# Kernel tuning notes

Measured on AMD Instinct MI355X. Metric: run time of the kernel, lower is better.

## Reference

```python
import jax, jax.numpy as jnp
import numpy as np

EPS = 1e-7  # tf.keras.backend.epsilon()
NUM_HEADS = 8


def setup_inputs() -> dict:
    key = jax.random.key(0)
    ks = jax.random.split(key, 7)
    B, H, W, C = 4, 128, 128, 512
    glorot = (2.0 / (C + C)) ** 0.5
    x = jax.random.normal(ks[0], (B, H, W, C), dtype=jnp.float32)
    wq = jax.random.normal(ks[1], (C, C), dtype=jnp.float32) * glorot
    bq = jnp.zeros((C,), dtype=jnp.float32)
    wk = jax.random.normal(ks[2], (C, C), dtype=jnp.float32) * glorot
    bk = jnp.zeros((C,), dtype=jnp.float32)
    wv = jax.random.normal(ks[3], (C, C), dtype=jnp.float32) * glorot
    bv = jnp.zeros((C,), dtype=jnp.float32)
    return {"x": x, "wq": wq, "bq": bq, "wk": wk, "bk": bk, "wv": wv, "bv": bv}


def _axial_attention(query, key, value, num_heads):
    B, H, W, C = value.shape
    d = query.shape[-1] // num_heads
    q5 = query.reshape(B, H, W, num_heads, d)
    k5 = key.reshape(B, H, W, num_heads, d)
    # column (vertical) attention: scores over H, per column w -> [B, nh, W, H, H]
    v_att = jnp.einsum("bhwnd,bgwnd->bnwhg", q5, k5)
    # row (horizontal) attention: scores over W, per row h -> [B, nh, H, W, W]
    u_att = jnp.einsum("bhwnd,bhvnd->bnhwv", q5, k5)
    # faithful clip-before-softmax chain from the original module
    v_att = jnp.clip(v_att, -1.0 + EPS, 1.0 - EPS)
    u_att = jnp.clip(u_att, -1.0 + EPS, 1.0 - EPS)
    scale = jnp.sqrt(jnp.asarray(d, dtype=v_att.dtype))
    v_att = v_att / scale
    u_att = u_att / scale
    # safed_softmax: softmax in fp32 (inputs already fp32 here)
    v_att = jax.nn.softmax(v_att.astype(jnp.float32), axis=-1).astype(query.dtype)
    u_att = jax.nn.softmax(u_att.astype(jnp.float32), axis=-1).astype(query.dtype)
    v_att = jnp.where(jnp.isnan(v_att), EPS, v_att)
    u_att = jnp.where(jnp.isnan(u_att), EPS, u_att)
    v_att = jnp.clip(v_att, EPS, 1.0 - EPS)
    u_att = jnp.clip(u_att, EPS, 1.0 - EPS)
    # value: [B, nh, W, H, d]
    val5 = value.reshape(B, H, W, num_heads, d)
    xv = jnp.einsum("bnwhg,bnwgd->bnhwd", v_att, val5.transpose(0, 3, 2, 1, 4))
    xu = jnp.einsum("bnhwv,bnhvd->bnhwd", u_att, xv)
    # transpose (0,2,3,4,1): head index becomes last -> channels ordered [d, nh]
    out = xu.transpose(0, 2, 3, 4, 1).reshape(B, H, W, d * num_heads)
    return out


def reference(x, wq, bq, wk, bk, wv, bv):
    # 1x1 convs == per-pixel dense projections
    query = jnp.einsum("bhwc,cf->bhwf", x, wq) + bq
    key = jnp.einsum("bhwc,cf->bhwf", x, wk) + bk
    value = jnp.einsum("bhwc,cf->bhwf", x, wv) + bv
    return _axial_attention(query, key, value, NUM_HEADS)
```

## Files before the change

kernel.cpp:

```cpp
#include <hip/hip_runtime.h>

typedef unsigned short ush;
typedef __attribute__((ext_vector_type(8))) __bf16 bf16x8;
typedef __attribute__((ext_vector_type(4))) float f32x4;

#define NE 33554432L

__device__ __forceinline__ float b2f(ush u) {
  return __uint_as_float(((unsigned int)u) << 16);
}
__device__ __forceinline__ ush f2b(float f) {
  unsigned int x = __float_as_uint(f);
  x += 0x7fffu + ((x >> 16) & 1u);
  return (ush)(x >> 16);
}
__device__ __forceinline__ bf16x8 bc8(int4 v) { return __builtin_bit_cast(bf16x8, v); }

__device__ __forceinline__ void gload16(const ush* g, ush* l) {
  __builtin_amdgcn_global_load_lds(
      (const __attribute__((address_space(1))) void*)g,
      (__attribute__((address_space(3))) void*)l, 16, 0, 0);
}

__global__ __launch_bounds__(256)
void detect_dtype(const ush* __restrict__ x, int* __restrict__ flag) {
  __shared__ int red[256];
  const int t = threadIdx.x;
  int cnt = 0;
  for (int i = t; i < 16384; i += 256) {
    const int e = (x[i] >> 7) & 0xFF;
    cnt += (e == 0 || (e >= 100 && e <= 142)) ? 1 : 0;
  }
  red[t] = cnt;
  __syncthreads();
  for (int s = 128; s > 0; s >>= 1) {
    if (t < s) red[t] += red[t + s];
    __syncthreads();
  }
  if (t == 0) flag[0] = (red[0] >= 13107) ? 1 : 0;
}

__global__ __launch_bounds__(256)
void pack_x(const void* __restrict__ xin, ush* __restrict__ xb,
            const int* __restrict__ flag) {
  const long i0 = ((long)blockIdx.x * 256 + threadIdx.x) * 8;
  if (*flag) {
    *(int4*)&xb[i0] = *(const int4*)&((const ush*)xin)[i0];
  } else {
    const float* xf = (const float*)xin;
    const float4 a = *(const float4*)&xf[i0];
    const float4 b = *(const float4*)&xf[i0 + 4];
    union { ush u[8]; int4 v; } r;
    r.u[0] = f2b(a.x); r.u[1] = f2b(a.y); r.u[2] = f2b(a.z); r.u[3] = f2b(a.w);
    r.u[4] = f2b(b.x); r.u[5] = f2b(b.y); r.u[6] = f2b(b.z); r.u[7] = f2b(b.w);
    *(int4*)&xb[i0] = r.v;
  }
}

__global__ __launch_bounds__(256)
void pack_w(const void* __restrict__ w0, const void* __restrict__ w1,
            const void* __restrict__ w2, ush* __restrict__ wTb,
            const int* __restrict__ flag) {
  __shared__ ush tile[32][33];
  const void* w = (blockIdx.z == 0) ? w0 : ((blockIdx.z == 1) ? w1 : w2);
  ush* wT = wTb + (long)blockIdx.z * 262144;
  const int bx = blockIdx.x * 32, by = blockIdx.y * 32;
  const int tx = threadIdx.x & 31, ty = threadIdx.x >> 5;
  const int f = *flag;
#pragma unroll
  for (int j = 0; j < 32; j += 8) {
    const int k = by + ty + j, n = bx + tx;
    tile[ty + j][tx] = f ? ((const ush*)w)[k * 512 + n]
                         : f2b(((const float*)w)[k * 512 + n]);
  }
  __syncthreads();
#pragma unroll
  for (int j = 0; j < 32; j += 8)
    wT[(bx + ty + j) * 512 + by + tx] = tile[tx][ty + j];
}

__global__ void pack_bias(const void* __restrict__ b0, const void* __restrict__ b1,
                          const void* __restrict__ b2, float* __restrict__ biasf,
                          const int* __restrict__ flag) {
  const void* b = (blockIdx.x == 0) ? b0 : ((blockIdx.x == 1) ? b1 : b2);
  const int n = threadIdx.x;
  const float v = (*flag) ? b2f(((const ush*)b)[n]) : ((const float*)b)[n];
  biasf[blockIdx.x * 512 + n] = v;
}

__global__ __launch_bounds__(256)
void proj_gemm(const ush* __restrict__ xb, const ush* __restrict__ wTb,
               const float* __restrict__ biasf, ush* __restrict__ qkv) {
  __shared__ ush As[4096];
  __shared__ ush Bs[4096];

  const int z = blockIdx.z;
  const ush* wt = wTb + (long)z * 262144;
  const float* bias = biasf + z * 512;
  ush* out = qkv + (long)z * NE;

  const int t = threadIdx.x;
  const int lane = t & 63;
  const int wvid = t >> 6;
  const int wm = wvid & 1, wn = wvid >> 1;
  const int col = lane & 15, quad = lane >> 4;

  const long m0 = (long)blockIdx.y * 128;
  const int n0 = blockIdx.x * 128;

  const int r_in_g = lane >> 2;
  const int swz = (((lane & 3) ^ ((r_in_g >> 1) & 3)) * 8);
  const int g0 = wvid * 2, g1 = g0 + 1;
  const ush* gA0 = xb + (m0 + g0 * 16 + r_in_g) * 512 + swz;
  const ush* gA1 = xb + (m0 + g1 * 16 + r_in_g) * 512 + swz;
  const ush* gB0 = wt + (long)(n0 + g0 * 16 + r_in_g) * 512 + swz;
  const ush* gB1 = wt + (long)(n0 + g1 * 16 + r_in_g) * 512 + swz;
  ush* lA0 = &As[g0 * 512];
  ush* lA1 = &As[g1 * 512];
  ush* lB0 = &Bs[g0 * 512];
  ush* lB1 = &Bs[g1 * 512];

  const int kswz = ((quad ^ ((col >> 1) & 3)) * 8);
  int aofs[4], bofs[4];
#pragma unroll
  for (int i = 0; i < 4; i++) aofs[i] = (wm * 64 + i * 16 + col) * 32 + kswz;
#pragma unroll
  for (int j = 0; j < 4; j++) bofs[j] = (wn * 64 + j * 16 + col) * 32 + kswz;

  const f32x4 z4 = {0.f, 0.f, 0.f, 0.f};
  f32x4 acc[4][4];
#pragma unroll
  for (int i = 0; i < 4; i++)
#pragma unroll
    for (int j = 0; j < 4; j++) acc[i][j] = z4;

  for (int k0 = 0; k0 < 512; k0 += 32) {
    gload16(gA0 + k0, lA0);
    gload16(gA1 + k0, lA1);
    gload16(gB0 + k0, lB0);
    gload16(gB1 + k0, lB1);
    __syncthreads();
    bf16x8 a[4], b[4];
#pragma unroll
    for (int i = 0; i < 4; i++) a[i] = bc8(*(const int4*)&As[aofs[i]]);
#pragma unroll
    for (int j = 0; j < 4; j++) b[j] = bc8(*(const int4*)&Bs[bofs[j]]);
#pragma unroll
    for (int i = 0; i < 4; i++)
#pragma unroll
      for (int j = 0; j < 4; j++)
        acc[i][j] = __builtin_amdgcn_mfma_f32_16x16x32_bf16(a[i], b[j], acc[i][j], 0, 0, 0);
    __syncthreads();
  }

#pragma unroll
  for (int j = 0; j < 4; j++) {
    const int n = n0 + wn * 64 + j * 16 + col;
    const float bb = bias[n];
#pragma unroll
    for (int i = 0; i < 4; i++) {
      const long row0 = m0 + wm * 64 + i * 16 + quad * 4;
#pragma unroll
      for (int r = 0; r < 4; r++)
        out[(row0 + r) * 512 + n] = f2b(acc[i][j][r] + bb);
    }
  }
}

#define QS_STRIDE 72
#define VT_STRIDE 136
#define P_STRIDE  136

__device__ __forceinline__ int vt_idx(int d, int g) {
  return d * VT_STRIDE + ((((g >> 3) ^ ((d >> 3) & 7)) << 3) | (g & 7));
}

template<int PASS>
__global__ __launch_bounds__(256, 3)
void axial_attn_mfma(const ush* __restrict__ Qb, const ush* __restrict__ Kb,
                     ush* __restrict__ Vb, void* __restrict__ outp,
                     const int* __restrict__ flagp) {
  __shared__ ush smem[27136];
  ush* Qs = smem;
  ush* Ks = smem + 9216;
  ush* Vt = smem + 18432;
  ush* P  = smem;

  const int flg = *flagp;
  const int b = blockIdx.z, n = blockIdx.y, pp = blockIdx.x;
  long base; int stride;
  if (PASS == 1) { base = ((long)b * 16384 + pp) * 512 + n * 64; stride = 65536; }
  else           { base = ((long)(b * 128 + pp) * 128) * 512 + n * 64; stride = 512; }

  const int t = threadIdx.x;
#pragma unroll
  for (int it = 0; it < 4; it++) {
    const int c = t + it * 256;
    const int row = c >> 3, c8 = c & 7;
    const long g = base + (long)row * stride + c8 * 8;
    int4 q = *(const int4*)(Qb + g);
    int4 k = *(const int4*)(Kb + g);
    int4 v = *(const int4*)(Vb + g);
    *(int4*)&Qs[row * QS_STRIDE + c8 * 8] = q;
    *(int4*)&Ks[row * QS_STRIDE + c8 * 8] = k;
    union { int4 i4; ush u[8]; } vu; vu.i4 = v;
#pragma unroll
    for (int dd = 0; dd < 8; dd++)
      Vt[vt_idx(c8 * 8 + dd, row)] = vu.u[dd];
  }
  __syncthreads();

  const int lane = t & 63, wv = t >> 6;
  const int col = lane & 15, quad = lane >> 4;
  const int m0 = wv * 32;
  const f32x4 z4 = {0.f, 0.f, 0.f, 0.f};

  f32x4 sacc[2][8];
#pragma unroll
  for (int i = 0; i < 2; i++)
#pragma unroll
    for (int j = 0; j < 8; j++) sacc[i][j] = z4;
#pragma unroll
  for (int k0 = 0; k0 < 64; k0 += 32) {
    bf16x8 a[2], kb[8];
#pragma unroll
    for (int i = 0; i < 2; i++)
      a[i] = bc8(*(const int4*)&Qs[(m0 + i * 16 + col) * QS_STRIDE + k0 + quad * 8]);
#pragma unroll
    for (int j = 0; j < 8; j++)
      kb[j] = bc8(*(const int4*)&Ks[(j * 16 + col) * QS_STRIDE + k0 + quad * 8]);
#pragma unroll
    for (int i = 0; i < 2; i++)
#pragma unroll
      for (int j = 0; j < 8; j++)
        sacc[i][j] = __builtin_amdgcn_mfma_f32_16x16x32_bf16(a[i], kb[j], sacc[i][j], 0, 0, 0);
  }

  const float CLIP = 1.0f - 1e-7f;
  float e[2][8][4], inv[2][4];
#pragma unroll
  for (int i = 0; i < 2; i++)
#pragma unroll
    for (int r = 0; r < 4; r++) {
      float part = 0.f;
#pragma unroll
      for (int j = 0; j < 8; j++) {
        float s = sacc[i][j][r];
        s = fminf(fmaxf(s, -CLIP), CLIP) * 0.125f;
        const float ee = __expf(s);
        e[i][j][r] = ee;
        part += ee;
      }
      part += __shfl_xor(part, 1);
      part += __shfl_xor(part, 2);
      part += __shfl_xor(part, 4);
      part += __shfl_xor(part, 8);
      inv[i][r] = 1.0f / part;
    }
  __syncthreads();

#pragma unroll
  for (int i = 0; i < 2; i++)
#pragma unroll
    for (int r = 0; r < 4; r++) {
      const int row = m0 + i * 16 + quad * 4 + r;
#pragma unroll
      for (int j = 0; j < 8; j++) {
        const float pv = fminf(fmaxf(e[i][j][r] * inv[i][r], 1e-7f), CLIP);
        P[row * P_STRIDE + j * 16 + col] = f2b(pv);
      }
    }
  __syncthreads();

  f32x4 oacc[2][4];
#pragma unroll
  for (int i = 0; i < 2; i++)
#pragma unroll
    for (int j = 0; j < 4; j++) oacc[i][j] = z4;
#pragma unroll
  for (int k0 = 0; k0 < 128; k0 += 32) {
    bf16x8 a[2], vb[4];
#pragma unroll
    for (int i = 0; i < 2; i++)
      a[i] = bc8(*(const int4*)&P[(m0 + i * 16 + col) * P_STRIDE + k0 + quad * 8]);
#pragma unroll
    for (int j = 0; j < 4; j++)
      vb[j] = bc8(*(const int4*)&Vt[vt_idx(j * 16 + col, k0 + quad * 8)]);
#pragma unroll
    for (int i = 0; i < 2; i++)
#pragma unroll
      for (int j = 0; j < 4; j++)
        oacc[i][j] = __builtin_amdgcn_mfma_f32_16x16x32_bf16(a[i], vb[j], oacc[i][j], 0, 0, 0);
  }

#pragma unroll
  for (int i = 0; i < 2; i++)
#pragma unroll
    for (int r = 0; r < 4; r++) {
      const int row = m0 + i * 16 + quad * 4 + r;
#pragma unroll
      for (int j = 0; j < 4; j++) {
        const int d = j * 16 + col;
        const float val = oacc[i][j][r];
        if (PASS == 1) {
          Vb[base + (long)row * stride + d] = f2b(val);
        } else {
          const long oi = ((long)(b * 128 + pp) * 128 + row) * 512 + d * 8 + n;
          if (flg) ((ush*)outp)[oi] = f2b(val);
          else     ((float*)outp)[oi] = val;
        }
      }
    }
}

extern "C" void kernel_launch(void* const* d_in, const int* in_sizes, int n_in,
                              void* d_out, int out_size, void* d_ws, size_t ws_size,
                              hipStream_t stream) {
  const void* x  = d_in[0];
  const void* wq = d_in[1];
  const void* bq = d_in[2];
  const void* wk = d_in[3];
  const void* bk = d_in[4];
  const void* wv = d_in[5];
  const void* bv = d_in[6];

  char* ws = (char*)d_ws;
  int*   flag  = (int*)ws;
  float* biasf = (float*)(ws + 256);
  ush*   wTb   = (ush*)(ws + 8192);
  ush*   xb    = (ush*)(ws + 8192 + 1572864);
  ush*   qkv   = (ush*)(ws + 8192 + 1572864 + 67108864);

  dim3 blk(256);
  detect_dtype<<<1, blk, 0, stream>>>((const ush*)x, flag);
  pack_bias<<<3, 512, 0, stream>>>(bq, bk, bv, biasf, flag);
  pack_w<<<dim3(16, 16, 3), blk, 0, stream>>>(wq, wk, wv, wTb, flag);
  pack_x<<<16384, blk, 0, stream>>>(x, xb, flag);

  ush* Q = qkv;
  ush* K = Q + NE;
  ush* V = K + NE;
  proj_gemm<<<dim3(4, 512, 3), blk, 0, stream>>>(xb, wTb, biasf, Q);
  dim3 agrid(128, 8, 4);
  axial_attn_mfma<1><<<agrid, blk, 0, stream>>>(Q, K, V, d_out, flag);
  axial_attn_mfma<2><<<agrid, blk, 0, stream>>>(Q, K, V, d_out, flag);
}
```

Baseline: 681.3 us.

## Double-buffer projection GEMM, coalesce attention stores, add output interleave kernel

The projection GEMM now double-buffers its LDS tiles and prefetches the next K slice while the current one is being multiplied. The attention kernel raises wave priority around its MFMA loops. Pass 1 stages its output through LDS so V is written with coalesced 16-byte stores. Pass 2 writes a contiguous fp32 scratch tensor, reusing the xb workspace, and a new out_interleave kernel transposes it into the strided [d, nh] channel layout through LDS, processed in two batch halves. This targets the scattered per-element output writes at the cost of extra scratch traffic and more kernel launches.

```diff
diff --git a/kernel.cpp b/kernel.cpp
--- a/kernel.cpp
+++ b/kernel.cpp
@@ -91,8 +91,8 @@
 __global__ __launch_bounds__(256)
 void proj_gemm(const ush* __restrict__ xb, const ush* __restrict__ wTb,
                const float* __restrict__ biasf, ush* __restrict__ qkv) {
-  __shared__ ush As[4096];
-  __shared__ ush Bs[4096];
+  __shared__ ush As[2][4096];
+  __shared__ ush Bs[2][4096];
 
   const int z = blockIdx.z;
   const ush* wt = wTb + (long)z * 262144;
@@ -115,17 +115,13 @@
   const ush* gA1 = xb + (m0 + g1 * 16 + r_in_g) * 512 + swz;
   const ush* gB0 = wt + (long)(n0 + g0 * 16 + r_in_g) * 512 + swz;
   const ush* gB1 = wt + (long)(n0 + g1 * 16 + r_in_g) * 512 + swz;
-  ush* lA0 = &As[g0 * 512];
-  ush* lA1 = &As[g1 * 512];
-  ush* lB0 = &Bs[g0 * 512];
-  ush* lB1 = &Bs[g1 * 512];
 
   const int kswz = ((quad ^ ((col >> 1) & 3)) * 8);
-  int aofs[4], bofs[4];
+  int aofs[4], bofs4[4];
 #pragma unroll
   for (int i = 0; i < 4; i++) aofs[i] = (wm * 64 + i * 16 + col) * 32 + kswz;
 #pragma unroll
-  for (int j = 0; j < 4; j++) bofs[j] = (wn * 64 + j * 16 + col) * 32 + kswz;
+  for (int j = 0; j < 4; j++) bofs4[j] = (wn * 64 + j * 16 + col) * 32 + kswz;
 
   const f32x4 z4 = {0.f, 0.f, 0.f, 0.f};
   f32x4 acc[4][4];
@@ -134,23 +130,34 @@
 #pragma unroll
     for (int j = 0; j < 4; j++) acc[i][j] = z4;
 
+  gload16(gA0, &As[0][g0 * 512]);
+  gload16(gA1, &As[0][g1 * 512]);
+  gload16(gB0, &Bs[0][g0 * 512]);
+  gload16(gB1, &Bs[0][g1 * 512]);
+  __syncthreads();
+
+  int cur = 0;
   for (int k0 = 0; k0 < 512; k0 += 32) {
-    gload16(gA0 + k0, lA0);
-    gload16(gA1 + k0, lA1);
-    gload16(gB0 + k0, lB0);
-    gload16(gB1 + k0, lB1);
-    __syncthreads();
+    const int nk = k0 + 32;
+    if (nk < 512) {
+      const int nb = cur ^ 1;
+      gload16(gA0 + nk, &As[nb][g0 * 512]);
+      gload16(gA1 + nk, &As[nb][g1 * 512]);
+      gload16(gB0 + nk, &Bs[nb][g0 * 512]);
+      gload16(gB1 + nk, &Bs[nb][g1 * 512]);
+    }
     bf16x8 a[4], b[4];
 #pragma unroll
-    for (int i = 0; i < 4; i++) a[i] = bc8(*(const int4*)&As[aofs[i]]);
-#pragma unroll
-    for (int j = 0; j < 4; j++) b[j] = bc8(*(const int4*)&Bs[bofs[j]]);
+    for (int i = 0; i < 4; i++) a[i] = bc8(*(const int4*)&As[cur][aofs[i]]);
+#pragma unroll
+    for (int j = 0; j < 4; j++) b[j] = bc8(*(const int4*)&Bs[cur][bofs4[j]]);
 #pragma unroll
     for (int i = 0; i < 4; i++)
 #pragma unroll
       for (int j = 0; j < 4; j++)
         acc[i][j] = __builtin_amdgcn_mfma_f32_16x16x32_bf16(a[i], b[j], acc[i][j], 0, 0, 0);
     __syncthreads();
+    cur ^= 1;
   }
 
 #pragma unroll
@@ -170,6 +177,7 @@
 #define QS_STRIDE 72
 #define VT_STRIDE 136
 #define P_STRIDE  136
+#define OS_STRIDE 72
 
 __device__ __forceinline__ int vt_idx(int d, int g) {
   return d * VT_STRIDE + ((((g >> 3) ^ ((d >> 3) & 7)) << 3) | (g & 7));
@@ -178,16 +186,15 @@
 template<int PASS>
 __global__ __launch_bounds__(256, 3)
 void axial_attn_mfma(const ush* __restrict__ Qb, const ush* __restrict__ Kb,
-                     ush* __restrict__ Vb, void* __restrict__ outp,
-                     const int* __restrict__ flagp) {
+                     ush* __restrict__ Vb, float* __restrict__ xuf,
+                     const int bofs) {
   __shared__ ush smem[27136];
   ush* Qs = smem;
   ush* Ks = smem + 9216;
   ush* Vt = smem + 18432;
   ush* P  = smem;
 
-  const int flg = *flagp;
-  const int b = blockIdx.z, n = blockIdx.y, pp = blockIdx.x;
+  const int b = blockIdx.z + bofs, n = blockIdx.y, pp = blockIdx.x;
   long base; int stride;
   if (PASS == 1) { base = ((long)b * 16384 + pp) * 512 + n * 64; stride = 65536; }
   else           { base = ((long)(b * 128 + pp) * 128) * 512 + n * 64; stride = 512; }
@@ -220,6 +227,7 @@
   for (int i = 0; i < 2; i++)
 #pragma unroll
     for (int j = 0; j < 8; j++) sacc[i][j] = z4;
+  __builtin_amdgcn_s_setprio(1);
 #pragma unroll
   for (int k0 = 0; k0 < 64; k0 += 32) {
     bf16x8 a[2], kb[8];
@@ -235,6 +243,7 @@
       for (int j = 0; j < 8; j++)
         sacc[i][j] = __builtin_amdgcn_mfma_f32_16x16x32_bf16(a[i], kb[j], sacc[i][j], 0, 0, 0);
   }
+  __builtin_amdgcn_s_setprio(0);
 
   const float CLIP = 1.0f - 1e-7f;
   float e[2][8][4], inv[2][4];
@@ -277,6 +286,7 @@
   for (int i = 0; i < 2; i++)
 #pragma unroll
     for (int j = 0; j < 4; j++) oacc[i][j] = z4;
+  __builtin_amdgcn_s_setprio(1);
 #pragma unroll
   for (int k0 = 0; k0 < 128; k0 += 32) {
     bf16x8 a[2], vb[4];
@@ -292,25 +302,81 @@
       for (int j = 0; j < 4; j++)
         oacc[i][j] = __builtin_amdgcn_mfma_f32_16x16x32_bf16(a[i], vb[j], oacc[i][j], 0, 0, 0);
   }
-
-#pragma unroll
-  for (int i = 0; i < 2; i++)
-#pragma unroll
-    for (int r = 0; r < 4; r++) {
-      const int row = m0 + i * 16 + quad * 4 + r;
-#pragma unroll
-      for (int j = 0; j < 4; j++) {
-        const int d = j * 16 + col;
-        const float val = oacc[i][j][r];
-        if (PASS == 1) {
-          Vb[base + (long)row * stride + d] = f2b(val);
-        } else {
-          const long oi = ((long)(b * 128 + pp) * 128 + row) * 512 + d * 8 + n;
-          if (flg) ((ush*)outp)[oi] = f2b(val);
-          else     ((float*)outp)[oi] = val;
-        }
+  __builtin_amdgcn_s_setprio(0);
+
+  if (PASS == 1) {
+    __syncthreads();
+    ush* Os = smem;
+#pragma unroll
+    for (int i = 0; i < 2; i++)
+#pragma unroll
+      for (int r = 0; r < 4; r++) {
+        const int row = m0 + i * 16 + quad * 4 + r;
+#pragma unroll
+        for (int j = 0; j < 4; j++)
+          Os[row * OS_STRIDE + j * 16 + col] = f2b(oacc[i][j][r]);
       }
-    }
+    __syncthreads();
+#pragma unroll
+    for (int it = 0; it < 4; it++) {
+      const int g2 = t + it * 256;
+      const int row = g2 >> 3, c8 = g2 & 7;
+      *(int4*)&Vb[base + (long)row * stride + c8 * 8] =
+          *(const int4*)&Os[row * OS_STRIDE + c8 * 8];
+    }
+  } else {
+    const long xbase = (((long)(blockIdx.z * 8 + n) * 128 + pp) * 128) * 64;
+#pragma unroll
+    for (int i = 0; i < 2; i++)
+#pragma unroll
+      for (int r = 0; r < 4; r++) {
+        const int row = m0 + i * 16 + quad * 4 + r;
+#pragma unroll
+        for (int j = 0; j < 4; j++)
+          xuf[xbase + (long)row * 64 + j * 16 + col] = oacc[i][j][r];
+      }
+  }
+}
+
+__global__ __launch_bounds__(256)
+void out_interleave(const float* __restrict__ xu, void* __restrict__ outp,
+                    const int* __restrict__ flagp, const int bofs) {
+  __shared__ float lds[8192];
+  const int bz = blockIdx.z, h = blockIdx.y, w0 = blockIdx.x * 16;
+  const int t = threadIdx.x;
+#pragma unroll
+  for (int n = 0; n < 8; n++) {
+    const float* src = xu + ((((long)(bz * 8 + n)) * 128 + h) * 128 + w0) * 64;
+    const int e = t * 4, w = e >> 6, d = e & 63;
+    const float4 v = *(const float4*)&src[e];
+    const int dr = (d + n * 8) & 63;
+    *(float4*)&lds[(n * 16 + w) * 64 + dr] = v;
+  }
+  __syncthreads();
+  const int flg = *flagp;
+  const long obase = (((long)(bz + bofs) * 128 + h) * 128 + w0) * 512;
+  const int tc = t & 127, c0 = tc * 4;
+  const int d = c0 >> 3, n0 = c0 & 7;
+#pragma unroll
+  for (int ro = 0; ro < 8; ro++) {
+    const int w = (t >> 7) * 8 + ro;
+    float r[4];
+#pragma unroll
+    for (int k = 0; k < 4; k++) {
+      const int n = n0 + k;
+      r[k] = lds[(n * 16 + w) * 64 + ((d + n * 8) & 63)];
+    }
+    const long oi = obase + (long)w * 512 + c0;
+    if (flg) {
+      union { ush u[4]; int2 v; } o;
+      o.u[0] = f2b(r[0]); o.u[1] = f2b(r[1]);
+      o.u[2] = f2b(r[2]); o.u[3] = f2b(r[3]);
+      *(int2*)&((ush*)outp)[oi] = o.v;
+    } else {
+      float4 o; o.x = r[0]; o.y = r[1]; o.z = r[2]; o.w = r[3];
+      *(float4*)&((float*)outp)[oi] = o;
+    }
+  }
 }
 
 extern "C" void kernel_launch(void* const* d_in, const int* in_sizes, int n_in,
@@ -329,6 +395,7 @@
   float* biasf = (float*)(ws + 256);
   ush*   wTb   = (ush*)(ws + 8192);
   ush*   xb    = (ush*)(ws + 8192 + 1572864);
+  float* xuf   = (float*)(ws + 8192 + 1572864);
   ush*   qkv   = (ush*)(ws + 8192 + 1572864 + 67108864);
 
   dim3 blk(256);
@@ -341,7 +408,9 @@
   ush* K = Q + NE;
   ush* V = K + NE;
   proj_gemm<<<dim3(4, 512, 3), blk, 0, stream>>>(xb, wTb, biasf, Q);
-  dim3 agrid(128, 8, 4);
-  axial_attn_mfma<1><<<agrid, blk, 0, stream>>>(Q, K, V, d_out, flag);
-  axial_attn_mfma<2><<<agrid, blk, 0, stream>>>(Q, K, V, d_out, flag);
-}
+  axial_attn_mfma<1><<<dim3(128, 8, 4), blk, 0, stream>>>(Q, K, V, nullptr, 0);
+  for (int half = 0; half < 2; half++) {
+    axial_attn_mfma<2><<<dim3(128, 8, 2), blk, 0, stream>>>(Q, K, V, xuf, half * 2);
+    out_interleave<<<dim3(8, 128, 2), blk, 0, stream>>>(xuf, d_out, flag, half * 2);
+  }
+}
```

Measured after the change: 590.0 us. -13.4%, faster.
